# Kernel tuning notes

Hardware: AMD Instinct MI355X
Metric: run time of the kernel (lower is better)

Reference implementation:

```python
import jax, jax.numpy as jnp
import numpy as np
import math

M, DIN, DTGT = 65536, 256, 256   # feature count and feature dims
S, SD_IN, SD_TGT = 64, 256, 256  # num_slots, in_slot_dim, tgt_slot_dim
ITERS = 3
H_IN = 128                        # mlp_in hidden (hardcoded 128 in source)
H_TGT = SD_TGT if SD_TGT > 128 else 128  # mlp_tgt hidden

ARGS = ["inputs", "target", "in_slots", "tgt_slots",
        "ln_in_g", "ln_in_b", "ln_tgt_g", "ln_tgt_b",
        "Wk", "bk", "Wv", "bv", "Wvt", "bvt",
        "ln_slots_g", "ln_slots_b", "Wq", "bq",
        "gru_in_Wih", "gru_in_Whh", "gru_in_bih", "gru_in_bhh",
        "gru_tgt_Wih", "gru_tgt_Whh", "gru_tgt_bih", "gru_tgt_bhh",
        "ln_mi_g", "ln_mi_b", "mi_W1", "mi_b1", "mi_W2", "mi_b2",
        "ln_mt_g", "ln_mt_b", "mt_W1", "mt_b1", "mt_W2", "mt_b2"]


def _ln(x, g, b):
    m = jnp.mean(x, axis=-1, keepdims=True)
    v = jnp.var(x, axis=-1, keepdims=True)
    return (x - m) * jax.lax.rsqrt(v + 1e-5) * g + b


def _gru(x, h, Wih, Whh, bih, bhh):
    # torch.nn.GRUCell semantics; Wih: (D, 3H), Whh: (H, 3H)
    H = h.shape[-1]
    gi = x @ Wih + bih
    gh = h @ Whh + bhh
    r = jax.nn.sigmoid(gi[:, :H] + gh[:, :H])
    z = jax.nn.sigmoid(gi[:, H:2 * H] + gh[:, H:2 * H])
    n = jnp.tanh(gi[:, 2 * H:] + r * gh[:, 2 * H:])
    return (1.0 - z) * n + z * h


def _forward(inputs, target, in_slots, tgt_slots,
             ln_in_g, ln_in_b, ln_tgt_g, ln_tgt_b,
             Wk, bk, Wv, bv, Wvt, bvt,
             ln_slots_g, ln_slots_b, Wq, bq,
             gru_in_Wih, gru_in_Whh, gru_in_bih, gru_in_bhh,
             gru_tgt_Wih, gru_tgt_Whh, gru_tgt_bih, gru_tgt_bhh,
             ln_mi_g, ln_mi_b, mi_W1, mi_b1, mi_W2, mi_b2,
             ln_mt_g, ln_mt_b, mt_W1, mt_b1, mt_W2, mt_b2):
    inputs_norm = _ln(inputs, ln_in_g, ln_in_b)          # [M, DIN]
    in_k = inputs_norm @ Wk + bk                          # [M, SD_IN]
    in_v = inputs_norm @ Wv + bv                          # [M, SD_IN]
    tgt_v = _ln(target, ln_tgt_g, ln_tgt_b) @ Wvt + bvt   # [M, SD_TGT]
    scale = 1.0 / math.sqrt(in_k.shape[1])
    attn = None
    for _ in range(ITERS):
        q = _ln(in_slots, ln_slots_g, ln_slots_b) @ Wq + bq   # [S, SD_IN]
        logits = (q @ in_k.T) * scale                          # [S, M]
        attn = jax.nn.softmax(logits, axis=0)                  # softmax over SLOTS (dim=0)
        in_up = attn @ in_v                                    # [S, SD_IN]
        tgt_up = attn @ tgt_v                                  # [S, SD_TGT]
        in_slots = _gru(in_up, in_slots, gru_in_Wih, gru_in_Whh, gru_in_bih, gru_in_bhh)
        tgt_slots = _gru(tgt_up, tgt_slots, gru_tgt_Wih, gru_tgt_Whh, gru_tgt_bih, gru_tgt_bhh)
        in_slots = in_slots + (jax.nn.relu(_ln(in_slots, ln_mi_g, ln_mi_b) @ mi_W1 + mi_b1) @ mi_W2 + mi_b2)
        tgt_slots = tgt_slots + (jax.nn.relu(_ln(tgt_slots, ln_mt_g, ln_mt_b) @ mt_W1 + mt_b1) @ mt_W2 + mt_b2)
    return (in_slots, tgt_slots, attn)


def setup_inputs() -> dict:
    key = jax.random.key(0)
    ks = iter(jax.random.split(key, 64))
    rn = lambda shape, s=1.0: jax.random.normal(next(ks), shape, dtype=jnp.float32) * s
    w = 0.02
    d = {
        "inputs": rn((M, DIN)),
        "target": rn((M, DTGT)),
        "in_slots": rn((S, SD_IN)),
        "tgt_slots": rn((S, SD_TGT)),
        "ln_in_g": jnp.ones((DIN,)), "ln_in_b": jnp.zeros((DIN,)),
        "ln_tgt_g": jnp.ones((DTGT,)), "ln_tgt_b": jnp.zeros((DTGT,)),
        "Wk": rn((DIN, SD_IN), w), "bk": jnp.zeros((SD_IN,)),
        "Wv": rn((DIN, SD_IN), w), "bv": jnp.zeros((SD_IN,)),
        "Wvt": rn((DTGT, SD_TGT), w), "bvt": jnp.zeros((SD_TGT,)),
        "ln_slots_g": jnp.ones((SD_IN,)), "ln_slots_b": jnp.zeros((SD_IN,)),
        "Wq": rn((SD_IN, SD_IN), w), "bq": jnp.zeros((SD_IN,)),
        "gru_in_Wih": rn((SD_IN, 3 * SD_IN), w), "gru_in_Whh": rn((SD_IN, 3 * SD_IN), w),
        "gru_in_bih": jnp.zeros((3 * SD_IN,)), "gru_in_bhh": jnp.zeros((3 * SD_IN,)),
        "gru_tgt_Wih": rn((SD_TGT, 3 * SD_TGT), w), "gru_tgt_Whh": rn((SD_TGT, 3 * SD_TGT), w),
        "gru_tgt_bih": jnp.zeros((3 * SD_TGT,)), "gru_tgt_bhh": jnp.zeros((3 * SD_TGT,)),
        "ln_mi_g": jnp.ones((SD_IN,)), "ln_mi_b": jnp.zeros((SD_IN,)),
        "mi_W1": rn((SD_IN, H_IN), w), "mi_b1": jnp.zeros((H_IN,)),
        "mi_W2": rn((H_IN, SD_IN), w), "mi_b2": jnp.zeros((SD_IN,)),
        "ln_mt_g": jnp.ones((SD_TGT,)), "ln_mt_b": jnp.zeros((SD_TGT,)),
        "mt_W1": rn((SD_TGT, H_TGT), w), "mt_b1": jnp.zeros((H_TGT,)),
        "mt_W2": rn((H_TGT, SD_TGT), w), "mt_b2": jnp.zeros((SD_TGT,)),
    }
    return {k: d[k] for k in ARGS}


def reference(inputs, target, in_slots, tgt_slots,
              ln_in_g, ln_in_b, ln_tgt_g, ln_tgt_b,
              Wk, bk, Wv, bv, Wvt, bvt,
              ln_slots_g, ln_slots_b, Wq, bq,
              gru_in_Wih, gru_in_Whh, gru_in_bih, gru_in_bhh,
              gru_tgt_Wih, gru_tgt_Whh, gru_tgt_bih, gru_tgt_bhh,
              ln_mi_g, ln_mi_b, mi_W1, mi_b1, mi_W2, mi_b2,
              ln_mt_g, ln_mt_b, mt_W1, mt_b1, mt_W2, mt_b2):
    return _forward(inputs, target, in_slots, tgt_slots,
                    ln_in_g, ln_in_b, ln_tgt_g, ln_tgt_b,
                    Wk, bk, Wv, bv, Wvt, bvt,
                    ln_slots_g, ln_slots_b, Wq, bq,
                    gru_in_Wih, gru_in_Whh, gru_in_bih, gru_in_bhh,
                    gru_tgt_Wih, gru_tgt_Whh, gru_tgt_bih, gru_tgt_bhh,
                    ln_mi_g, ln_mi_b, mi_W1, mi_b1, mi_W2, mi_b2,
                    ln_mt_g, ln_mt_b, mt_W1, mt_b1, mt_W2, mt_b2)
```

## Files before the change

### kernel.cpp

```cpp
#include <hip/hip_runtime.h>
#include <hip/hip_bf16.h>
#include <math.h>

typedef __bf16 bf16_t;
typedef __bf16 bf16x8 __attribute__((ext_vector_type(8)));
typedef float f32x4 __attribute__((ext_vector_type(4)));

#define DEVI __device__ __forceinline__

DEVI f32x4 mfma16(bf16x8 a, bf16x8 b, f32x4 c) {
  return __builtin_amdgcn_mfma_f32_16x16x32_bf16(a, b, c, 0, 0, 0);
}
DEVI bf16x8 ld8(const bf16_t* p) { return *reinterpret_cast<const bf16x8*>(p); }

struct WtArgs { const float* s0; const float* s1; const float* s2; const float* s3;
                const float* s4; const float* s5; const float* s6; const float* s7;
                const float* s8; const float* s9; const float* s10; const float* s11; };

__global__ __launch_bounds__(256) void k_wtrans(WtArgs A, bf16_t* __restrict__ wt) {
  constexpr int offs[13] = {0,65536,131072,196608,262144,458752,655360,851968,
                            1048576,1081344,1114112,1179648,1245184};
  constexpr int Ks[12]   = {256,256,256,256,256,256,256,256,256,128,256,256};
  constexpr int Ns[12]   = {256,256,256,256,768,768,768,768,128,256,256,256};
  int gid = blockIdx.x * 256 + threadIdx.x;
  if (gid >= 1245184) return;
  int mi = 0;
  #pragma unroll
  for (int i = 1; i < 12; ++i) if (gid >= offs[i]) mi = i;
  const int i0 = gid - offs[mi];
  const int K = Ks[mi], N = Ns[mi];
  int n, k;
  if (K == 256) { n = i0 >> 8; k = i0 & 255; } else { n = i0 >> 7; k = i0 & 127; }
  const float* sp;
  switch (mi) {
    case 0: sp = A.s0; break; case 1: sp = A.s1; break; case 2: sp = A.s2; break;
    case 3: sp = A.s3; break; case 4: sp = A.s4; break; case 5: sp = A.s5; break;
    case 6: sp = A.s6; break; case 7: sp = A.s7; break; case 8: sp = A.s8; break;
    case 9: sp = A.s9; break; case 10: sp = A.s10; break; default: sp = A.s11; break;
  }
  wt[gid] = (bf16_t)(sp[(size_t)k * N + n]);
}

__global__ __launch_bounds__(256) void k_init(const float* __restrict__ in_slots,
                                              const float* __restrict__ tgt_slots,
                                              float* __restrict__ h_f32,
                                              bf16_t* __restrict__ h_bf) {
  int idx = blockIdx.x * 256 + threadIdx.x;
  int side = idx >> 14, j = idx & 16383;
  float x = (side ? tgt_slots : in_slots)[j];
  h_f32[idx] = x;
  h_bf[idx] = (bf16_t)x;
}

__global__ __launch_bounds__(256) void k_phaseA(
    const float* __restrict__ inputs, const float* __restrict__ target,
    const float* __restrict__ ln_in_g, const float* __restrict__ ln_in_b,
    const float* __restrict__ ln_tgt_g, const float* __restrict__ ln_tgt_b,
    const bf16_t* __restrict__ wkT, const bf16_t* __restrict__ wvT, const bf16_t* __restrict__ wvtT,
    const float* __restrict__ bk, const float* __restrict__ bv, const float* __restrict__ bvt,
    bf16_t* __restrict__ in_k, bf16_t* __restrict__ in_vT, bf16_t* __restrict__ tgt_vT) {
  const int side = blockIdx.y;
  const int m0 = blockIdx.x * 64;
  const int t = threadIdx.x;
  __shared__ __align__(16) bf16_t anorm[64][264];
  __shared__ float gs[256], bs[256];
  {
    const float* g = side ? ln_tgt_g : ln_in_g;
    const float* bb = side ? ln_tgt_b : ln_in_b;
    gs[t] = g[t]; bs[t] = bb[t];
  }
  const float* src = side ? target : inputs;
  const int r = t >> 2, qd = t & 3;
  const float4* rowp = reinterpret_cast<const float4*>(src + (size_t)(m0 + r) * 256 + qd * 64);
  float v[64];
  float s1 = 0.f, s2 = 0.f;
  #pragma unroll
  for (int j = 0; j < 16; ++j) {
    float4 x = rowp[j];
    v[4*j+0] = x.x; v[4*j+1] = x.y; v[4*j+2] = x.z; v[4*j+3] = x.w;
    s1 += x.x + x.y + x.z + x.w;
    s2 += x.x*x.x + x.y*x.y + x.z*x.z + x.w*x.w;
  }
  s1 += __shfl_xor(s1, 1); s1 += __shfl_xor(s1, 2);
  s2 += __shfl_xor(s2, 1); s2 += __shfl_xor(s2, 2);
  const float mean = s1 * (1.f/256.f);
  const float var  = s2 * (1.f/256.f) - mean*mean;
  const float rstd = rsqrtf(var + 1e-5f);
  __syncthreads();
  #pragma unroll
  for (int j = 0; j < 64; ++j) {
    const int c = qd*64 + j;
    anorm[r][c] = (bf16_t)((v[j] - mean) * rstd * gs[c] + bs[c]);
  }
  __syncthreads();
  const int l = t & 63, w = t >> 6, l16 = l & 15, l4 = l >> 4;

  if (side == 0) {
    f32x4 acc[4][4] = {};
    for (int ks = 0; ks < 8; ++ks) {
      const int k = ks*32 + l4*8;
      bf16x8 a[4], b[4];
      #pragma unroll
      for (int mi = 0; mi < 4; ++mi) a[mi] = ld8(&anorm[mi*16 + l16][k]);
      #pragma unroll
      for (int ni = 0; ni < 4; ++ni) b[ni] = ld8(wkT + (size_t)(w*64 + ni*16 + l16)*256 + k);
      #pragma unroll
      for (int mi = 0; mi < 4; ++mi)
        #pragma unroll
        for (int ni = 0; ni < 4; ++ni) acc[mi][ni] = mfma16(a[mi], b[ni], acc[mi][ni]);
    }
    #pragma unroll
    for (int mi = 0; mi < 4; ++mi)
      #pragma unroll
      for (int ni = 0; ni < 4; ++ni) {
        const int d = w*64 + ni*16 + l16;
        const float bias = bk[d];
        #pragma unroll
        for (int rr = 0; rr < 4; ++rr) {
          const int m = m0 + mi*16 + l4*4 + rr;
          in_k[(size_t)m*256 + d] = (bf16_t)(acc[mi][ni][rr] + bias);
        }
      }
  }
  {
    const bf16_t* WT = side ? wvtT : wvT;
    const float* bias = side ? bvt : bv;
    bf16_t* out = side ? tgt_vT : in_vT;
    f32x4 acc[4][4] = {};
    for (int ks = 0; ks < 8; ++ks) {
      const int k = ks*32 + l4*8;
      bf16x8 a[4], b[4];
      #pragma unroll
      for (int mi = 0; mi < 4; ++mi) a[mi] = ld8(WT + (size_t)(w*64 + mi*16 + l16)*256 + k);
      #pragma unroll
      for (int ni = 0; ni < 4; ++ni) b[ni] = ld8(&anorm[ni*16 + l16][k]);
      #pragma unroll
      for (int mi = 0; mi < 4; ++mi)
        #pragma unroll
        for (int ni = 0; ni < 4; ++ni) acc[mi][ni] = mfma16(a[mi], b[ni], acc[mi][ni]);
    }
    #pragma unroll
    for (int mi = 0; mi < 4; ++mi)
      #pragma unroll
      for (int ni = 0; ni < 4; ++ni) {
        const int m = m0 + ni*16 + l16;
        #pragma unroll
        for (int rr = 0; rr < 4; ++rr) {
          const int d = w*64 + mi*16 + l4*4 + rr;
          out[(size_t)d*65536 + m] = (bf16_t)(acc[mi][ni][rr] + bias[d]);
        }
      }
  }
}

__global__ __launch_bounds__(256) void k_q(
    const float* __restrict__ h_in,
    const float* __restrict__ ln_g, const float* __restrict__ ln_b,
    const bf16_t* __restrict__ wqT, const float* __restrict__ bq,
    bf16_t* __restrict__ q_bf) {
  __shared__ __align__(16) bf16_t anorm[64][264];
  __shared__ float gs[256], bs[256];
  const int t = threadIdx.x;
  gs[t] = ln_g[t]; bs[t] = ln_b[t];
  const int r = t >> 2, qd = t & 3;
  const float4* rowp = reinterpret_cast<const float4*>(h_in + (size_t)r*256 + qd*64);
  float v[64];
  float s1 = 0.f, s2 = 0.f;
  #pragma unroll
  for (int j = 0; j < 16; ++j) {
    float4 x = rowp[j];
    v[4*j+0] = x.x; v[4*j+1] = x.y; v[4*j+2] = x.z; v[4*j+3] = x.w;
    s1 += x.x + x.y + x.z + x.w;
    s2 += x.x*x.x + x.y*x.y + x.z*x.z + x.w*x.w;
  }
  s1 += __shfl_xor(s1, 1); s1 += __shfl_xor(s1, 2);
  s2 += __shfl_xor(s2, 1); s2 += __shfl_xor(s2, 2);
  const float mean = s1 * (1.f/256.f);
  const float rstd = rsqrtf(s2 * (1.f/256.f) - mean*mean + 1e-5f);
  __syncthreads();
  #pragma unroll
  for (int j = 0; j < 64; ++j) {
    const int c = qd*64 + j;
    anorm[r][c] = (bf16_t)((v[j] - mean) * rstd * gs[c] + bs[c]);
  }
  __syncthreads();
  const int l = t & 63, w = t >> 6, l16 = l & 15, l4 = l >> 4;
  f32x4 acc[4][4] = {};
  for (int ks = 0; ks < 8; ++ks) {
    const int k = ks*32 + l4*8;
    bf16x8 a[4], b[4];
    #pragma unroll
    for (int mi = 0; mi < 4; ++mi) a[mi] = ld8(&anorm[mi*16 + l16][k]);
    #pragma unroll
    for (int ni = 0; ni < 4; ++ni) b[ni] = ld8(wqT + (size_t)(w*64 + ni*16 + l16)*256 + k);
    #pragma unroll
    for (int mi = 0; mi < 4; ++mi)
      #pragma unroll
      for (int ni = 0; ni < 4; ++ni) acc[mi][ni] = mfma16(a[mi], b[ni], acc[mi][ni]);
  }
  #pragma unroll
  for (int mi = 0; mi < 4; ++mi)
    #pragma unroll
    for (int ni = 0; ni < 4; ++ni) {
      const int d = w*64 + ni*16 + l16;
      const float bias = bq[d];
      #pragma unroll
      for (int rr = 0; rr < 4; ++rr) {
        const int s = mi*16 + l4*4 + rr;
        q_bf[(size_t)s*256 + d] = (bf16_t)((acc[mi][ni][rr] + bias) * 0.0625f);
      }
    }
}

__global__ __launch_bounds__(256) void k_logits(
    const bf16_t* __restrict__ q_bf, const bf16_t* __restrict__ in_k,
    bf16_t* __restrict__ attn_bf, float* __restrict__ attn_f32, int write_f32) {
  const int t = threadIdx.x, l = t & 63, w = t >> 6, l16 = l & 15, l4 = l >> 4;
  const int m0 = blockIdx.x * 256 + w * 64;
  f32x4 acc[4][4] = {};
  for (int ks = 0; ks < 8; ++ks) {
    const int k = ks*32 + l4*8;
    bf16x8 a[4], b[4];
    #pragma unroll
    for (int mi = 0; mi < 4; ++mi) a[mi] = ld8(q_bf + (size_t)(mi*16 + l16)*256 + k);
    #pragma unroll
    for (int ni = 0; ni < 4; ++ni) b[ni] = ld8(in_k + (size_t)(m0 + ni*16 + l16)*256 + k);
    #pragma unroll
    for (int mi = 0; mi < 4; ++mi)
      #pragma unroll
      for (int ni = 0; ni < 4; ++ni) acc[mi][ni] = mfma16(a[mi], b[ni], acc[mi][ni]);
  }
  #pragma unroll
  for (int ni = 0; ni < 4; ++ni) {
    float mx = -3.0e38f;
    #pragma unroll
    for (int mi = 0; mi < 4; ++mi)
      #pragma unroll
      for (int rr = 0; rr < 4; ++rr) mx = fmaxf(mx, acc[mi][ni][rr]);
    mx = fmaxf(mx, __shfl_xor(mx, 16));
    mx = fmaxf(mx, __shfl_xor(mx, 32));
    float sm = 0.f;
    #pragma unroll
    for (int mi = 0; mi < 4; ++mi)
      #pragma unroll
      for (int rr = 0; rr < 4; ++rr) {
        float e = __expf(acc[mi][ni][rr] - mx);
        acc[mi][ni][rr] = e; sm += e;
      }
    sm += __shfl_xor(sm, 16);
    sm += __shfl_xor(sm, 32);
    const float inv = 1.0f / sm;
    #pragma unroll
    for (int mi = 0; mi < 4; ++mi)
      #pragma unroll
      for (int rr = 0; rr < 4; ++rr) acc[mi][ni][rr] *= inv;
  }
  #pragma unroll
  for (int mi = 0; mi < 4; ++mi)
    #pragma unroll
    for (int ni = 0; ni < 4; ++ni)
      #pragma unroll
      for (int rr = 0; rr < 4; ++rr) {
        const int s = mi*16 + l4*4 + rr;
        const size_t idx = (size_t)s*65536 + (m0 + ni*16 + l16);
        attn_bf[idx] = (bf16_t)acc[mi][ni][rr];
        if (write_f32) attn_f32[idx] = acc[mi][ni][rr];
      }
}

__global__ __launch_bounds__(256) void k_pv(
    const bf16_t* __restrict__ attn_bf,
    const bf16_t* __restrict__ in_vT, const bf16_t* __restrict__ tgt_vT,
    float* __restrict__ p_in, float* __restrict__ p_tgt) {
  const int c = blockIdx.x, side = blockIdx.y;
  const bf16_t* V = side ? tgt_vT : in_vT;
  float* P = side ? p_tgt : p_in;
  const int t = threadIdx.x, l = t & 63, w = t >> 6, l16 = l & 15, l4 = l >> 4;
  f32x4 acc[4][4] = {};
  for (int ks = 0; ks < 16; ++ks) {
    const int km = c*512 + ks*32 + l4*8;
    bf16x8 a[4], b[4];
    #pragma unroll
    for (int mi = 0; mi < 4; ++mi) a[mi] = ld8(attn_bf + (size_t)(mi*16 + l16)*65536 + km);
    #pragma unroll
    for (int ni = 0; ni < 4; ++ni) b[ni] = ld8(V + (size_t)(w*64 + ni*16 + l16)*65536 + km);
    #pragma unroll
    for (int mi = 0; mi < 4; ++mi)
      #pragma unroll
      for (int ni = 0; ni < 4; ++ni) acc[mi][ni] = mfma16(a[mi], b[ni], acc[mi][ni]);
  }
  #pragma unroll
  for (int mi = 0; mi < 4; ++mi)
    #pragma unroll
    for (int ni = 0; ni < 4; ++ni) {
      const int d = w*64 + ni*16 + l16;
      #pragma unroll
      for (int rr = 0; rr < 4; ++rr) {
        const int s = mi*16 + l4*4 + rr;
        P[(size_t)c*16384 + s*256 + d] = acc[mi][ni][rr];
      }
    }
}

__global__ __launch_bounds__(256) void k_pvred(
    const float* __restrict__ p_in, const float* __restrict__ p_tgt,
    bf16_t* __restrict__ up_bf) {
  const int b = blockIdx.x;
  const int side = b >> 6, s = b & 63;
  const int d = threadIdx.x;
  const float* P = (side ? p_tgt : p_in) + s*256 + d;
  float sum = 0.f;
  #pragma unroll 8
  for (int cc = 0; cc < 128; ++cc) sum += P[(size_t)cc * 16384];
  up_bf[side*16384 + s*256 + d] = (bf16_t)sum;
}

__global__ __launch_bounds__(256) void k_gates(
    const bf16_t* __restrict__ up_bf, const bf16_t* __restrict__ h_bf,
    const bf16_t* __restrict__ wihT_in, const bf16_t* __restrict__ whhT_in,
    const bf16_t* __restrict__ wihT_tgt, const bf16_t* __restrict__ whhT_tgt,
    const float* __restrict__ bih_in, const float* __restrict__ bhh_in,
    const float* __restrict__ bih_tgt, const float* __restrict__ bhh_tgt,
    float* __restrict__ gi, float* __restrict__ gh) {
  const int nchunk = blockIdx.x, which = blockIdx.y, side = blockIdx.z;
  const bf16_t* Aop = (which ? h_bf : up_bf) + side*16384;
  const bf16_t* WT = side ? (which ? whhT_tgt : wihT_tgt) : (which ? whhT_in : wihT_in);
  const float* bias = side ? (which ? bhh_tgt : bih_tgt) : (which ? bhh_in : bih_in);
  float* out = (which ? gh : gi) + side*49152;
  const int t = threadIdx.x, l = t & 63, w = t >> 6, l16 = l & 15, l4 = l >> 4;
  const int n0 = nchunk*256 + w*64;
  f32x4 acc[4][4] = {};
  for (int ks = 0; ks < 8; ++ks) {
    const int k = ks*32 + l4*8;
    bf16x8 a[4], b[4];
    #pragma unroll
    for (int mi = 0; mi < 4; ++mi) a[mi] = ld8(Aop + (size_t)(mi*16 + l16)*256 + k);
    #pragma unroll
    for (int ni = 0; ni < 4; ++ni) b[ni] = ld8(WT + (size_t)(n0 + ni*16 + l16)*256 + k);
    #pragma unroll
    for (int mi = 0; mi < 4; ++mi)
      #pragma unroll
      for (int ni = 0; ni < 4; ++ni) acc[mi][ni] = mfma16(a[mi], b[ni], acc[mi][ni]);
  }
  #pragma unroll
  for (int mi = 0; mi < 4; ++mi)
    #pragma unroll
    for (int ni = 0; ni < 4; ++ni) {
      const int n = n0 + ni*16 + l16;
      const float bb = bias[n];
      #pragma unroll
      for (int rr = 0; rr < 4; ++rr) {
        const int s = mi*16 + l4*4 + rr;
        out[(size_t)s*768 + n] = acc[mi][ni][rr] + bb;
      }
    }
}

__global__ __launch_bounds__(256) void k_gru_ln(
    const float* __restrict__ gi, const float* __restrict__ gh,
    const float* __restrict__ h_f32,
    const float* __restrict__ ln_mi_g, const float* __restrict__ ln_mi_b,
    const float* __restrict__ ln_mt_g, const float* __restrict__ ln_mt_b,
    float* __restrict__ hp_f32, bf16_t* __restrict__ hpnorm_bf) {
  const int s = blockIdx.x, side = blockIdx.y;
  const int d = threadIdx.x;
  const float* GI = gi + side*49152 + s*768;
  const float* GH = gh + side*49152 + s*768;
  const float hv = h_f32[side*16384 + s*256 + d];
  const float rg = 1.f / (1.f + __expf(-(GI[d] + GH[d])));
  const float zg = 1.f / (1.f + __expf(-(GI[256 + d] + GH[256 + d])));
  const float ng = tanhf(GI[512 + d] + rg * GH[512 + d]);
  const float hp = (1.f - zg) * ng + zg * hv;
  float a = hp, b2 = hp * hp;
  #pragma unroll
  for (int msk = 1; msk < 64; msk <<= 1) { a += __shfl_xor(a, msk); b2 += __shfl_xor(b2, msk); }
  __shared__ float reda[4], redb[4];
  const int w = d >> 6, l = d & 63;
  if (l == 0) { reda[w] = a; redb[w] = b2; }
  __syncthreads();
  const float S1 = reda[0] + reda[1] + reda[2] + reda[3];
  const float S2 = redb[0] + redb[1] + redb[2] + redb[3];
  const float mean = S1 * (1.f/256.f);
  const float rstd = rsqrtf(S2 * (1.f/256.f) - mean*mean + 1e-5f);
  const float* g = side ? ln_mt_g : ln_mi_g;
  const float* bb = side ? ln_mt_b : ln_mi_b;
  const float nv = (hp - mean) * rstd * g[d] + bb[d];
  hp_f32[side*16384 + s*256 + d] = hp;
  hpnorm_bf[side*16384 + s*256 + d] = (bf16_t)nv;
}

__global__ __launch_bounds__(64) void k_mlp1(
    const bf16_t* __restrict__ hpnorm_bf,
    const bf16_t* __restrict__ w1T_in, const bf16_t* __restrict__ w1T_tgt,
    const float* __restrict__ b1_in, const float* __restrict__ b1_tgt,
    bf16_t* __restrict__ hidden_bf) {
  const int nchunk = blockIdx.x, side = blockIdx.y;
  const int NH = side ? 256 : 128;
  const int n0 = nchunk * 64;
  if (n0 >= NH) return;
  const bf16_t* Aop = hpnorm_bf + side*16384;
  const bf16_t* WT = side ? w1T_tgt : w1T_in;
  const float* bias = side ? b1_tgt : b1_in;
  const int l = threadIdx.x, l16 = l & 15, l4 = l >> 4;
  f32x4 acc[4][4] = {};
  for (int ks = 0; ks < 8; ++ks) {
    const int k = ks*32 + l4*8;
    bf16x8 a[4], b[4];
    #pragma unroll
    for (int mi = 0; mi < 4; ++mi) a[mi] = ld8(Aop + (size_t)(mi*16 + l16)*256 + k);
    #pragma unroll
    for (int ni = 0; ni < 4; ++ni) b[ni] = ld8(WT + (size_t)(n0 + ni*16 + l16)*256 + k);
    #pragma unroll
    for (int mi = 0; mi < 4; ++mi)
      #pragma unroll
      for (int ni = 0; ni < 4; ++ni) acc[mi][ni] = mfma16(a[mi], b[ni], acc[mi][ni]);
  }
  #pragma unroll
  for (int mi = 0; mi < 4; ++mi)
    #pragma unroll
    for (int ni = 0; ni < 4; ++ni) {
      const int n = n0 + ni*16 + l16;
      const float bb = bias[n];
      #pragma unroll
      for (int rr = 0; rr < 4; ++rr) {
        const int s = mi*16 + l4*4 + rr;
        hidden_bf[side*16384 + s*256 + n] = (bf16_t)fmaxf(acc[mi][ni][rr] + bb, 0.f);
      }
    }
}

__global__ __launch_bounds__(64) void k_mlp2(
    const bf16_t* __restrict__ hidden_bf,
    const bf16_t* __restrict__ w2T_in, const bf16_t* __restrict__ w2T_tgt,
    const float* __restrict__ b2_in, const float* __restrict__ b2_tgt,
    const float* __restrict__ hp_f32,
    float* __restrict__ h_f32, bf16_t* __restrict__ h_bf, float* __restrict__ slots_out) {
  const int nchunk = blockIdx.x, side = blockIdx.y;
  const int KH = side ? 256 : 128;
  const int nsteps = KH >> 5;
  const bf16_t* Aop = hidden_bf + side*16384;
  const bf16_t* WT = side ? w2T_tgt : w2T_in;
  const float* bias = side ? b2_tgt : b2_in;
  const int n0 = nchunk * 64;
  const int l = threadIdx.x, l16 = l & 15, l4 = l >> 4;
  f32x4 acc[4][4] = {};
  for (int ks = 0; ks < nsteps; ++ks) {
    const int k = ks*32 + l4*8;
    bf16x8 a[4], b[4];
    #pragma unroll
    for (int mi = 0; mi < 4; ++mi) a[mi] = ld8(Aop + (size_t)(mi*16 + l16)*256 + k);
    #pragma unroll
    for (int ni = 0; ni < 4; ++ni) b[ni] = ld8(WT + (size_t)(n0 + ni*16 + l16)*KH + k);
    #pragma unroll
    for (int mi = 0; mi < 4; ++mi)
      #pragma unroll
      for (int ni = 0; ni < 4; ++ni) acc[mi][ni] = mfma16(a[mi], b[ni], acc[mi][ni]);
  }
  #pragma unroll
  for (int mi = 0; mi < 4; ++mi)
    #pragma unroll
    for (int ni = 0; ni < 4; ++ni) {
      const int n = n0 + ni*16 + l16;
      const float bb = bias[n];
      #pragma unroll
      for (int rr = 0; rr < 4; ++rr) {
        const int s = mi*16 + l4*4 + rr;
        const int idx = side*16384 + s*256 + n;
        const float val = acc[mi][ni][rr] + bb + hp_f32[idx];
        h_f32[idx] = val;
        h_bf[idx] = (bf16_t)val;
        slots_out[idx] = val;
      }
    }
}

extern "C" void kernel_launch(void* const* d_in, const int* in_sizes, int n_in,
                              void* d_out, int out_size, void* d_ws, size_t ws_size,
                              hipStream_t stream) {
  (void)in_sizes; (void)n_in; (void)out_size; (void)ws_size;
  const float* inputs     = (const float*)d_in[0];
  const float* target     = (const float*)d_in[1];
  const float* in_slots   = (const float*)d_in[2];
  const float* tgt_slots  = (const float*)d_in[3];
  const float* ln_in_g    = (const float*)d_in[4];
  const float* ln_in_b    = (const float*)d_in[5];
  const float* ln_tgt_g   = (const float*)d_in[6];
  const float* ln_tgt_b   = (const float*)d_in[7];
  const float* Wk  = (const float*)d_in[8];
  const float* bk  = (const float*)d_in[9];
  const float* Wv  = (const float*)d_in[10];
  const float* bv  = (const float*)d_in[11];
  const float* Wvt = (const float*)d_in[12];
  const float* bvt = (const float*)d_in[13];
  const float* ln_slots_g = (const float*)d_in[14];
  const float* ln_slots_b = (const float*)d_in[15];
  const float* Wq  = (const float*)d_in[16];
  const float* bq  = (const float*)d_in[17];
  const float* gru_in_Wih  = (const float*)d_in[18];
  const float* gru_in_Whh  = (const float*)d_in[19];
  const float* gru_in_bih  = (const float*)d_in[20];
  const float* gru_in_bhh  = (const float*)d_in[21];
  const float* gru_tgt_Wih = (const float*)d_in[22];
  const float* gru_tgt_Whh = (const float*)d_in[23];
  const float* gru_tgt_bih = (const float*)d_in[24];
  const float* gru_tgt_bhh = (const float*)d_in[25];
  const float* ln_mi_g = (const float*)d_in[26];
  const float* ln_mi_b = (const float*)d_in[27];
  const float* mi_W1 = (const float*)d_in[28];
  const float* mi_b1 = (const float*)d_in[29];
  const float* mi_W2 = (const float*)d_in[30];
  const float* mi_b2 = (const float*)d_in[31];
  const float* ln_mt_g = (const float*)d_in[32];
  const float* ln_mt_b = (const float*)d_in[33];
  const float* mt_W1 = (const float*)d_in[34];
  const float* mt_b1 = (const float*)d_in[35];
  const float* mt_W2 = (const float*)d_in[36];
  const float* mt_b2 = (const float*)d_in[37];

  char* ws = (char*)d_ws;
  bf16_t* wt      = (bf16_t*)(ws);
  bf16_t* in_k    = (bf16_t*)(ws + 2490368ull);
  bf16_t* in_vT   = (bf16_t*)(ws + 36044800ull);
  bf16_t* tgt_vT  = (bf16_t*)(ws + 69599232ull);
  bf16_t* attn_bf = (bf16_t*)(ws + 103153664ull);
  bf16_t* q_bf    = (bf16_t*)(ws + 111542272ull);
  bf16_t* h_bf    = (bf16_t*)(ws + 111575040ull);
  bf16_t* up_bf   = (bf16_t*)(ws + 111640576ull);
  bf16_t* hpn_bf  = (bf16_t*)(ws + 111706112ull);
  bf16_t* hid_bf  = (bf16_t*)(ws + 111771648ull);
  float*  h_f32   = (float*)(ws + 111837184ull);
  float*  hp_f32  = (float*)(ws + 111968256ull);
  float*  gi      = (float*)(ws + 112099328ull);
  float*  gh      = (float*)(ws + 112492544ull);
  float*  p_in    = (float*)(ws + 112885760ull);
  float*  p_tgt   = (float*)(ws + 121274368ull);

  bf16_t* wkT = wt;
  bf16_t* wvT = wt + 65536;
  bf16_t* wvtT = wt + 131072;
  bf16_t* wqT = wt + 196608;
  bf16_t* wihT_in  = wt + 262144;
  bf16_t* whhT_in  = wt + 458752;
  bf16_t* wihT_tgt = wt + 655360;
  bf16_t* whhT_tgt = wt + 851968;
  bf16_t* w1T_in  = wt + 1048576;
  bf16_t* w2T_in  = wt + 1081344;
  bf16_t* w1T_tgt = wt + 1114112;
  bf16_t* w2T_tgt = wt + 1179648;

  float* attn_out = (float*)d_out + 32768;

  WtArgs wa = {Wk, Wv, Wvt, Wq, gru_in_Wih, gru_in_Whh, gru_tgt_Wih, gru_tgt_Whh,
               mi_W1, mi_W2, mt_W1, mt_W2};
  k_wtrans<<<4864, 256, 0, stream>>>(wa, wt);
  k_init<<<128, 256, 0, stream>>>(in_slots, tgt_slots, h_f32, h_bf);
  k_phaseA<<<dim3(1024, 2), 256, 0, stream>>>(inputs, target, ln_in_g, ln_in_b,
      ln_tgt_g, ln_tgt_b, wkT, wvT, wvtT, bk, bv, bvt, in_k, in_vT, tgt_vT);

  for (int it = 0; it < 3; ++it) {
    k_q<<<1, 256, 0, stream>>>(h_f32, ln_slots_g, ln_slots_b, wqT, bq, q_bf);
    k_logits<<<256, 256, 0, stream>>>(q_bf, in_k, attn_bf, attn_out, it == 2 ? 1 : 0);
    k_pv<<<dim3(128, 2), 256, 0, stream>>>(attn_bf, in_vT, tgt_vT, p_in, p_tgt);
    k_pvred<<<128, 256, 0, stream>>>(p_in, p_tgt, up_bf);
    k_gates<<<dim3(3, 2, 2), 256, 0, stream>>>(up_bf, h_bf, wihT_in, whhT_in,
        wihT_tgt, whhT_tgt, gru_in_bih, gru_in_bhh, gru_tgt_bih, gru_tgt_bhh, gi, gh);
    k_gru_ln<<<dim3(64, 2), 256, 0, stream>>>(gi, gh, h_f32, ln_mi_g, ln_mi_b,
        ln_mt_g, ln_mt_b, hp_f32, hpn_bf);
    k_mlp1<<<dim3(4, 2), 64, 0, stream>>>(hpn_bf, w1T_in, w1T_tgt, mi_b1, mt_b1, hid_bf);
    k_mlp2<<<dim3(4, 2), 64, 0, stream>>>(hid_bf, w2T_in, w2T_tgt, mi_b2, mt_b2,
        hp_f32, h_f32, h_bf, (float*)d_out);
  }
}
```

Baseline: 364.7 us.

## Fuse MLP layers with next-iteration query, tile weight transpose, bf16 PV partials

Merges mlp1, mlp2 and the next iteration's slot LayerNorm plus query projection into one kernel, keeping the hidden activations in shared memory. This removes several tiny launches per iteration. The weight transpose now goes through tiled shared memory so that global reads and writes are coalesced. PV partial sums are stored as bf16 to halve partial-buffer traffic, and the LayerNorm stores to shared memory are packed into 8-wide vectors. The bf16 partials lose precision in the 128-way reduction. The fused kernel also runs on only 2 blocks and applies a 1/16 scale to q, which assumes k_logits does not scale again.

```diff
diff --git a/kernel.cpp b/kernel.cpp
--- a/kernel.cpp
+++ b/kernel.cpp
@@ -4,6 +4,7 @@
 
 typedef __bf16 bf16_t;
 typedef __bf16 bf16x8 __attribute__((ext_vector_type(8)));
+typedef __bf16 bf16x4 __attribute__((ext_vector_type(4)));
 typedef float f32x4 __attribute__((ext_vector_type(4)));
 
 #define DEVI __device__ __forceinline__
@@ -18,27 +19,38 @@
                 const float* s8; const float* s9; const float* s10; const float* s11; };
 
 __global__ __launch_bounds__(256) void k_wtrans(WtArgs A, bf16_t* __restrict__ wt) {
-  constexpr int offs[13] = {0,65536,131072,196608,262144,458752,655360,851968,
-                            1048576,1081344,1114112,1179648,1245184};
+  constexpr int offs[12] = {0,65536,131072,196608,262144,458752,655360,851968,
+                            1048576,1081344,1114112,1179648};
   constexpr int Ks[12]   = {256,256,256,256,256,256,256,256,256,128,256,256};
   constexpr int Ns[12]   = {256,256,256,256,768,768,768,768,128,256,256,256};
-  int gid = blockIdx.x * 256 + threadIdx.x;
-  if (gid >= 1245184) return;
-  int mi = 0;
-  #pragma unroll
-  for (int i = 1; i < 12; ++i) if (gid >= offs[i]) mi = i;
-  const int i0 = gid - offs[mi];
-  const int K = Ks[mi], N = Ns[mi];
-  int n, k;
-  if (K == 256) { n = i0 >> 8; k = i0 & 255; } else { n = i0 >> 7; k = i0 & 127; }
+  const int m = blockIdx.y;
+  const int K = Ks[m], N = Ns[m];
+  const int tn = N >> 6;
+  const int tile = blockIdx.x;
+  if (tile >= (K >> 6) * tn) return;
+  const int tk = tile / tn, tc = tile - tk * tn;
   const float* sp;
-  switch (mi) {
+  switch (m) {
     case 0: sp = A.s0; break; case 1: sp = A.s1; break; case 2: sp = A.s2; break;
     case 3: sp = A.s3; break; case 4: sp = A.s4; break; case 5: sp = A.s5; break;
     case 6: sp = A.s6; break; case 7: sp = A.s7; break; case 8: sp = A.s8; break;
     case 9: sp = A.s9; break; case 10: sp = A.s10; break; default: sp = A.s11; break;
   }
-  wt[gid] = (bf16_t)(sp[(size_t)k * N + n]);
+  __shared__ float ts[64][65];
+  const int t = threadIdx.x, c = t & 63, rq = t >> 6;
+  const int k0 = tk * 64, n0 = tc * 64;
+  #pragma unroll
+  for (int i = 0; i < 16; ++i) {
+    const int r = rq * 16 + i;
+    ts[r][c] = sp[(size_t)(k0 + r) * N + n0 + c];
+  }
+  __syncthreads();
+  bf16_t* dst = wt + offs[m];
+  #pragma unroll
+  for (int i = 0; i < 16; ++i) {
+    const int nr = rq * 16 + i;
+    dst[(size_t)(n0 + nr) * K + k0 + c] = (bf16_t)ts[c][nr];
+  }
 }
 
 __global__ __launch_bounds__(256) void k_init(const float* __restrict__ in_slots,
@@ -88,9 +100,14 @@
   const float rstd = rsqrtf(var + 1e-5f);
   __syncthreads();
   #pragma unroll
-  for (int j = 0; j < 64; ++j) {
-    const int c = qd*64 + j;
-    anorm[r][c] = (bf16_t)((v[j] - mean) * rstd * gs[c] + bs[c]);
+  for (int j = 0; j < 8; ++j) {
+    bf16x8 pk;
+    #pragma unroll
+    for (int e = 0; e < 8; ++e) {
+      const int c = qd*64 + j*8 + e;
+      pk[e] = (bf16_t)((v[j*8+e] - mean) * rstd * gs[c] + bs[c]);
+    }
+    *reinterpret_cast<bf16x8*>(&anorm[r][qd*64 + j*8]) = pk;
   }
   __syncthreads();
   const int l = t & 63, w = t >> 6, l16 = l & 15, l4 = l >> 4;
@@ -179,9 +196,14 @@
   const float rstd = rsqrtf(s2 * (1.f/256.f) - mean*mean + 1e-5f);
   __syncthreads();
   #pragma unroll
-  for (int j = 0; j < 64; ++j) {
-    const int c = qd*64 + j;
-    anorm[r][c] = (bf16_t)((v[j] - mean) * rstd * gs[c] + bs[c]);
+  for (int j = 0; j < 8; ++j) {
+    bf16x8 pk;
+    #pragma unroll
+    for (int e = 0; e < 8; ++e) {
+      const int c = qd*64 + j*8 + e;
+      pk[e] = (bf16_t)((v[j*8+e] - mean) * rstd * gs[c] + bs[c]);
+    }
+    *reinterpret_cast<bf16x8*>(&anorm[r][qd*64 + j*8]) = pk;
   }
   __syncthreads();
   const int l = t & 63, w = t >> 6, l16 = l & 15, l4 = l >> 4;
@@ -271,10 +293,10 @@
 __global__ __launch_bounds__(256) void k_pv(
     const bf16_t* __restrict__ attn_bf,
     const bf16_t* __restrict__ in_vT, const bf16_t* __restrict__ tgt_vT,
-    float* __restrict__ p_in, float* __restrict__ p_tgt) {
+    bf16_t* __restrict__ p_in, bf16_t* __restrict__ p_tgt) {
   const int c = blockIdx.x, side = blockIdx.y;
   const bf16_t* V = side ? tgt_vT : in_vT;
-  float* P = side ? p_tgt : p_in;
+  bf16_t* P = side ? p_tgt : p_in;
   const int t = threadIdx.x, l = t & 63, w = t >> 6, l16 = l & 15, l4 = l >> 4;
   f32x4 acc[4][4] = {};
   for (int ks = 0; ks < 16; ++ks) {
@@ -297,21 +319,21 @@
       #pragma unroll
       for (int rr = 0; rr < 4; ++rr) {
         const int s = mi*16 + l4*4 + rr;
-        P[(size_t)c*16384 + s*256 + d] = acc[mi][ni][rr];
+        P[(size_t)c*16384 + s*256 + d] = (bf16_t)acc[mi][ni][rr];
       }
     }
 }
 
 __global__ __launch_bounds__(256) void k_pvred(
-    const float* __restrict__ p_in, const float* __restrict__ p_tgt,
+    const bf16_t* __restrict__ p_in, const bf16_t* __restrict__ p_tgt,
     bf16_t* __restrict__ up_bf) {
   const int b = blockIdx.x;
   const int side = b >> 6, s = b & 63;
   const int d = threadIdx.x;
-  const float* P = (side ? p_tgt : p_in) + s*256 + d;
+  const bf16_t* P = (side ? p_tgt : p_in) + s*256 + d;
   float sum = 0.f;
   #pragma unroll 8
-  for (int cc = 0; cc < 128; ++cc) sum += P[(size_t)cc * 16384];
+  for (int cc = 0; cc < 128; ++cc) sum += (float)P[(size_t)cc * 16384];
   up_bf[side*16384 + s*256 + d] = (bf16_t)sum;
 }
 
@@ -389,89 +411,123 @@
   hpnorm_bf[side*16384 + s*256 + d] = (bf16_t)nv;
 }
 
-__global__ __launch_bounds__(64) void k_mlp1(
-    const bf16_t* __restrict__ hpnorm_bf,
+__global__ __launch_bounds__(256) void k_mlpq(
+    const bf16_t* __restrict__ hpn_bf,
     const bf16_t* __restrict__ w1T_in, const bf16_t* __restrict__ w1T_tgt,
     const float* __restrict__ b1_in, const float* __restrict__ b1_tgt,
-    bf16_t* __restrict__ hidden_bf) {
-  const int nchunk = blockIdx.x, side = blockIdx.y;
-  const int NH = side ? 256 : 128;
-  const int n0 = nchunk * 64;
-  if (n0 >= NH) return;
-  const bf16_t* Aop = hpnorm_bf + side*16384;
-  const bf16_t* WT = side ? w1T_tgt : w1T_in;
-  const float* bias = side ? b1_tgt : b1_in;
-  const int l = threadIdx.x, l16 = l & 15, l4 = l >> 4;
-  f32x4 acc[4][4] = {};
-  for (int ks = 0; ks < 8; ++ks) {
-    const int k = ks*32 + l4*8;
-    bf16x8 a[4], b[4];
-    #pragma unroll
-    for (int mi = 0; mi < 4; ++mi) a[mi] = ld8(Aop + (size_t)(mi*16 + l16)*256 + k);
-    #pragma unroll
-    for (int ni = 0; ni < 4; ++ni) b[ni] = ld8(WT + (size_t)(n0 + ni*16 + l16)*256 + k);
-    #pragma unroll
-    for (int mi = 0; mi < 4; ++mi)
-      #pragma unroll
-      for (int ni = 0; ni < 4; ++ni) acc[mi][ni] = mfma16(a[mi], b[ni], acc[mi][ni]);
-  }
-  #pragma unroll
-  for (int mi = 0; mi < 4; ++mi)
-    #pragma unroll
-    for (int ni = 0; ni < 4; ++ni) {
-      const int n = n0 + ni*16 + l16;
-      const float bb = bias[n];
-      #pragma unroll
-      for (int rr = 0; rr < 4; ++rr) {
-        const int s = mi*16 + l4*4 + rr;
-        hidden_bf[side*16384 + s*256 + n] = (bf16_t)fmaxf(acc[mi][ni][rr] + bb, 0.f);
-      }
-    }
-}
-
-__global__ __launch_bounds__(64) void k_mlp2(
-    const bf16_t* __restrict__ hidden_bf,
     const bf16_t* __restrict__ w2T_in, const bf16_t* __restrict__ w2T_tgt,
     const float* __restrict__ b2_in, const float* __restrict__ b2_tgt,
     const float* __restrict__ hp_f32,
-    float* __restrict__ h_f32, bf16_t* __restrict__ h_bf, float* __restrict__ slots_out) {
-  const int nchunk = blockIdx.x, side = blockIdx.y;
-  const int KH = side ? 256 : 128;
-  const int nsteps = KH >> 5;
-  const bf16_t* Aop = hidden_bf + side*16384;
-  const bf16_t* WT = side ? w2T_tgt : w2T_in;
-  const float* bias = side ? b2_tgt : b2_in;
-  const int n0 = nchunk * 64;
-  const int l = threadIdx.x, l16 = l & 15, l4 = l >> 4;
-  f32x4 acc[4][4] = {};
-  for (int ks = 0; ks < nsteps; ++ks) {
-    const int k = ks*32 + l4*8;
-    bf16x8 a[4], b[4];
-    #pragma unroll
-    for (int mi = 0; mi < 4; ++mi) a[mi] = ld8(Aop + (size_t)(mi*16 + l16)*256 + k);
-    #pragma unroll
-    for (int ni = 0; ni < 4; ++ni) b[ni] = ld8(WT + (size_t)(n0 + ni*16 + l16)*KH + k);
-    #pragma unroll
-    for (int mi = 0; mi < 4; ++mi)
-      #pragma unroll
-      for (int ni = 0; ni < 4; ++ni) acc[mi][ni] = mfma16(a[mi], b[ni], acc[mi][ni]);
-  }
-  #pragma unroll
-  for (int mi = 0; mi < 4; ++mi)
-    #pragma unroll
-    for (int ni = 0; ni < 4; ++ni) {
-      const int n = n0 + ni*16 + l16;
-      const float bb = bias[n];
-      #pragma unroll
-      for (int rr = 0; rr < 4; ++rr) {
-        const int s = mi*16 + l4*4 + rr;
-        const int idx = side*16384 + s*256 + n;
-        const float val = acc[mi][ni][rr] + bb + hp_f32[idx];
-        h_f32[idx] = val;
-        h_bf[idx] = (bf16_t)val;
-        slots_out[idx] = val;
-      }
-    }
+    float* __restrict__ h_f32, bf16_t* __restrict__ h_bf, float* __restrict__ slots_out,
+    const float* __restrict__ ln_sg, const float* __restrict__ ln_sb,
+    const bf16_t* __restrict__ wqT, const float* __restrict__ bq,
+    bf16_t* __restrict__ q_bf, int make_q) {
+  const int side = blockIdx.x;
+  __shared__ __align__(16) bf16_t hid[64][264];
+  const int t = threadIdx.x, l = t & 63, w = t >> 6, l16 = l & 15, l4 = l >> 4;
+  const int NH = side ? 256 : 128;
+  {
+    const bf16_t* Aop = hpn_bf + side*16384;
+    const bf16_t* WT = side ? w1T_tgt : w1T_in;
+    const float* b1 = side ? b1_tgt : b1_in;
+    const int ntiles = NH >> 6;
+    for (int nt = 0; nt < ntiles; ++nt) {
+      const int n0 = w*(NH>>2) + nt*16;
+      f32x4 acc[4] = {};
+      for (int ks = 0; ks < 8; ++ks) {
+        const int k = ks*32 + l4*8;
+        bf16x8 b = ld8(WT + (size_t)(n0 + l16)*256 + k);
+        #pragma unroll
+        for (int mt = 0; mt < 4; ++mt)
+          acc[mt] = mfma16(ld8(Aop + (size_t)(mt*16 + l16)*256 + k), b, acc[mt]);
+      }
+      const float bb = b1[n0 + l16];
+      #pragma unroll
+      for (int mt = 0; mt < 4; ++mt)
+        #pragma unroll
+        for (int rr = 0; rr < 4; ++rr) {
+          const int s = mt*16 + l4*4 + rr;
+          hid[s][n0 + l16] = (bf16_t)fmaxf(acc[mt][rr] + bb, 0.f);
+        }
+    }
+  }
+  __syncthreads();
+  {
+    const bf16_t* WT = side ? w2T_tgt : w2T_in;
+    const float* b2 = side ? b2_tgt : b2_in;
+    const int ksteps = NH >> 5;
+    #pragma unroll
+    for (int nt = 0; nt < 4; ++nt) {
+      const int n0 = w*64 + nt*16;
+      f32x4 acc[4] = {};
+      for (int ks = 0; ks < ksteps; ++ks) {
+        const int k = ks*32 + l4*8;
+        bf16x8 b = ld8(WT + (size_t)(n0 + l16)*NH + k);
+        #pragma unroll
+        for (int mt = 0; mt < 4; ++mt)
+          acc[mt] = mfma16(ld8(&hid[mt*16 + l16][k]), b, acc[mt]);
+      }
+      const int n = n0 + l16;
+      const float bb = b2[n];
+      #pragma unroll
+      for (int mt = 0; mt < 4; ++mt)
+        #pragma unroll
+        for (int rr = 0; rr < 4; ++rr) {
+          const int s = mt*16 + l4*4 + rr;
+          const int idx = side*16384 + s*256 + n;
+          const float val = acc[mt][rr] + bb + hp_f32[idx];
+          h_f32[idx] = val;
+          h_bf[idx] = (bf16_t)val;
+          slots_out[idx] = val;
+        }
+    }
+  }
+  if (!make_q || side != 0) return;
+  __syncthreads();
+  {
+    for (int i = 0; i < 16; ++i) {
+      const int s = w*16 + i;
+      float4 x = *reinterpret_cast<const float4*>(h_f32 + s*256 + 4*l);
+      float a = x.x + x.y + x.z + x.w;
+      float b2s = x.x*x.x + x.y*x.y + x.z*x.z + x.w*x.w;
+      #pragma unroll
+      for (int msk = 1; msk < 64; msk <<= 1) { a += __shfl_xor(a, msk); b2s += __shfl_xor(b2s, msk); }
+      const float mean = a * (1.f/256.f);
+      const float rstd = rsqrtf(b2s * (1.f/256.f) - mean*mean + 1e-5f);
+      float4 g4 = *reinterpret_cast<const float4*>(ln_sg + 4*l);
+      float4 bb4 = *reinterpret_cast<const float4*>(ln_sb + 4*l);
+      bf16x4 pk;
+      pk[0] = (bf16_t)((x.x - mean) * rstd * g4.x + bb4.x);
+      pk[1] = (bf16_t)((x.y - mean) * rstd * g4.y + bb4.y);
+      pk[2] = (bf16_t)((x.z - mean) * rstd * g4.z + bb4.z);
+      pk[3] = (bf16_t)((x.w - mean) * rstd * g4.w + bb4.w);
+      *reinterpret_cast<bf16x4*>(&hid[s][4*l]) = pk;
+    }
+  }
+  __syncthreads();
+  {
+    #pragma unroll
+    for (int nt = 0; nt < 4; ++nt) {
+      const int n0 = w*64 + nt*16;
+      f32x4 acc[4] = {};
+      for (int ks = 0; ks < 8; ++ks) {
+        const int k = ks*32 + l4*8;
+        bf16x8 b = ld8(wqT + (size_t)(n0 + l16)*256 + k);
+        #pragma unroll
+        for (int mt = 0; mt < 4; ++mt)
+          acc[mt] = mfma16(ld8(&hid[mt*16 + l16][k]), b, acc[mt]);
+      }
+      const int d = n0 + l16;
+      const float bb = bq[d];
+      #pragma unroll
+      for (int mt = 0; mt < 4; ++mt)
+        #pragma unroll
+        for (int rr = 0; rr < 4; ++rr) {
+          const int s = mt*16 + l4*4 + rr;
+          q_bf[(size_t)s*256 + d] = (bf16_t)((acc[mt][rr] + bb) * 0.0625f);
+        }
+    }
+  }
 }
 
 extern "C" void kernel_launch(void* const* d_in, const int* in_sizes, int n_in,
@@ -526,14 +582,13 @@
   bf16_t* q_bf    = (bf16_t*)(ws + 111542272ull);
   bf16_t* h_bf    = (bf16_t*)(ws + 111575040ull);
   bf16_t* up_bf   = (bf16_t*)(ws + 111640576ull);
-  bf16_t* hpn_bf  = (bf16_t*)(ws + 111706112ull);
-  bf16_t* hid_bf  = (bf16_t*)(ws + 111771648ull);
-  float*  h_f32   = (float*)(ws + 111837184ull);
-  float*  hp_f32  = (float*)(ws + 111968256ull);
-  float*  gi      = (float*)(ws + 112099328ull);
-  float*  gh      = (float*)(ws + 112492544ull);
-  float*  p_in    = (float*)(ws + 112885760ull);
-  float*  p_tgt   = (float*)(ws + 121274368ull);
+  bf16_t* hpn_bf  = (bf16_t*)(ws + 111673344ull);
+  float*  h_f32   = (float*)(ws + 111706112ull);
+  float*  hp_f32  = (float*)(ws + 111837184ull);
+  float*  gi      = (float*)(ws + 111968256ull);
+  float*  gh      = (float*)(ws + 112361472ull);
+  bf16_t* p_in    = (bf16_t*)(ws + 112754688ull);
+  bf16_t* p_tgt   = (bf16_t*)(ws + 116948992ull);
 
   bf16_t* wkT = wt;
   bf16_t* wvT = wt + 65536;
@@ -552,13 +607,13 @@
 
   WtArgs wa = {Wk, Wv, Wvt, Wq, gru_in_Wih, gru_in_Whh, gru_tgt_Wih, gru_tgt_Whh,
                mi_W1, mi_W2, mt_W1, mt_W2};
-  k_wtrans<<<4864, 256, 0, stream>>>(wa, wt);
+  k_wtrans<<<dim3(48, 12), 256, 0, stream>>>(wa, wt);
   k_init<<<128, 256, 0, stream>>>(in_slots, tgt_slots, h_f32, h_bf);
   k_phaseA<<<dim3(1024, 2), 256, 0, stream>>>(inputs, target, ln_in_g, ln_in_b,
       ln_tgt_g, ln_tgt_b, wkT, wvT, wvtT, bk, bv, bvt, in_k, in_vT, tgt_vT);
+  k_q<<<1, 256, 0, stream>>>(h_f32, ln_slots_g, ln_slots_b, wqT, bq, q_bf);
 
   for (int it = 0; it < 3; ++it) {
-    k_q<<<1, 256, 0, stream>>>(h_f32, ln_slots_g, ln_slots_b, wqT, bq, q_bf);
     k_logits<<<256, 256, 0, stream>>>(q_bf, in_k, attn_bf, attn_out, it == 2 ? 1 : 0);
     k_pv<<<dim3(128, 2), 256, 0, stream>>>(attn_bf, in_vT, tgt_vT, p_in, p_tgt);
     k_pvred<<<128, 256, 0, stream>>>(p_in, p_tgt, up_bf);
@@ -566,8 +621,8 @@
         wihT_tgt, whhT_tgt, gru_in_bih, gru_in_bhh, gru_tgt_bih, gru_tgt_bhh, gi, gh);
     k_gru_ln<<<dim3(64, 2), 256, 0, stream>>>(gi, gh, h_f32, ln_mi_g, ln_mi_b,
         ln_mt_g, ln_mt_b, hp_f32, hpn_bf);
-    k_mlp1<<<dim3(4, 2), 64, 0, stream>>>(hpn_bf, w1T_in, w1T_tgt, mi_b1, mt_b1, hid_bf);
-    k_mlp2<<<dim3(4, 2), 64, 0, stream>>>(hid_bf, w2T_in, w2T_tgt, mi_b2, mt_b2,
-        hp_f32, h_f32, h_bf, (float*)d_out);
-  }
-}
+    k_mlpq<<<2, 256, 0, stream>>>(hpn_bf, w1T_in, w1T_tgt, mi_b1, mt_b1,
+        w2T_in, w2T_tgt, mi_b2, mt_b2, hp_f32, h_f32, h_bf, (float*)d_out,
+        ln_slots_g, ln_slots_b, wqT, bq, q_bf, it < 2 ? 1 : 0);
+  }
+}
```

Measured after the change: 352.3 us. -3.4%, faster.
